# Kernel tuning notes

Measured on AMD Instinct MI355X. Metric: run time of the kernel, lower is better.

## Reference

```python
import jax, jax.numpy as jnp
import numpy as np

B, C, CI, H, W = 8, 256, 128, 64, 64
EPS = 1e-5

def conv1x1(x, w, b):
    # x: [B,C,H,W], w: [O,C], b: [O]
    return jnp.einsum('bchw,oc->bohw', x, w) + b[None, :, None, None]

def avgpool2(x):
    b, c, h, w = x.shape
    return x.reshape(b, c, h // 2, 2, w // 2, 2).mean(axis=(3, 5))

def setup_inputs() -> dict:
    key = jax.random.key(0)
    ks = jax.random.split(key, 16)
    s = lambda fan: 1.0 / np.sqrt(fan)
    inp = {
        'q': jax.random.normal(ks[0], (B, C, H, W), jnp.float32),
        'k': jax.random.normal(ks[1], (B, C, H, W), jnp.float32),
        'v': jax.random.normal(ks[2], (B, C, H, W), jnp.float32),
        'Wg':  jax.random.normal(ks[3], (CI, C), jnp.float32) * s(C),
        'bg':  jax.random.normal(ks[4], (CI,), jnp.float32) * s(C),
        'Wth': jax.random.normal(ks[5], (CI, C), jnp.float32) * s(C),
        'bth': jax.random.normal(ks[6], (CI,), jnp.float32) * s(C),
        'Wph': jax.random.normal(ks[7], (CI, C), jnp.float32) * s(C),
        'bph': jax.random.normal(ks[8], (CI,), jnp.float32) * s(C),
        'Ww':  jax.random.normal(ks[9], (C, CI), jnp.float32) * s(CI),
        'bw':  jax.random.normal(ks[10], (C,), jnp.float32) * s(CI),
        'gamma': jax.random.normal(ks[11], (C,), jnp.float32) * 0.1 + 1.0,
        'beta':  jax.random.normal(ks[12], (C,), jnp.float32) * 0.1,
        'mean':  jax.random.normal(ks[13], (C,), jnp.float32) * 0.1,
        'var':   jax.random.uniform(ks[14], (C,), jnp.float32, 0.5, 1.5),
    }
    return inp

def reference(q, k, v, Wg, bg, Wth, bth, Wph, bph, Ww, bw, gamma, beta, mean, var):
    b = q.shape[0]
    # g branch on v, phi branch on q: 1x1 conv then 2x2 avg-pool (sub_sample)
    g_x = avgpool2(conv1x1(v, Wg, bg)).reshape(b, CI, -1)            # [B,CI,M]
    g_x = g_x.transpose(0, 2, 1)                                      # [B,M,CI]
    theta_x = conv1x1(k, Wth, bth).reshape(b, CI, -1).transpose(0, 2, 1)  # [B,N,CI]
    phi_x = avgpool2(conv1x1(q, Wph, bph)).reshape(b, CI, -1)        # [B,CI,M]
    f = jnp.einsum('bnc,bcm->bnm', theta_x, phi_x)                   # [B,N,M]
    f_div_C = jax.nn.softmax(f, axis=-1)
    y = jnp.einsum('bnm,bmc->bnc', f_div_C, g_x)                     # [B,N,CI]
    y = y.transpose(0, 2, 1).reshape(b, CI, H, W)
    W_y = conv1x1(y, Ww, bw)
    # BatchNorm2d (inference form)
    W_y = (W_y - mean[None, :, None, None]) * (gamma[None, :, None, None]
            * jax.lax.rsqrt(var + EPS)[None, :, None, None]) + beta[None, :, None, None]
    return W_y + v
```

## Files before the change

### kernel.cpp

```cpp
#include <hip/hip_runtime.h>
#include <cstddef>

typedef unsigned short u16;
typedef unsigned int u32;
typedef __attribute__((ext_vector_type(8))) __bf16 bf16x8;
typedef __attribute__((ext_vector_type(4))) float f32x4;

constexpr int kB = 8, kC = 256, kCI = 128, kN = 4096, kM = 1024;
constexpr int kHM = 512;
constexpr int kCH = 32;
constexpr int kNCH = kHM / kCH;
constexpr float kEPS = 1e-5f;
constexpr float kLOG2E = 1.44269504088896f;

__device__ __forceinline__ u16 f2bf(float f) {
    u32 u = __float_as_uint(f);
    u32 r = (u + 0x7fffu + ((u >> 16) & 1u)) >> 16;
    return (u16)r;
}

__device__ __forceinline__ void gload_lds16(const u16* g, u16* l) {
    __builtin_amdgcn_global_load_lds(
        (const __attribute__((address_space(1))) void*)g,
        (__attribute__((address_space(3))) void*)l, 16, 0, 0);
}

__global__ __launch_bounds__(256) void prep_kernel(const float* __restrict__ Wth,
                                                   const float* __restrict__ bth,
                                                   const float* __restrict__ Wph,
                                                   const float* __restrict__ Wg,
                                                   const float* __restrict__ Ww,
                                                   const float* __restrict__ bw,
                                                   const float* __restrict__ gamma,
                                                   const float* __restrict__ beta,
                                                   const float* __restrict__ mean,
                                                   const float* __restrict__ var,
                                                   u16* __restrict__ Wthb,
                                                   u16* __restrict__ Wphb,
                                                   u16* __restrict__ Wgb,
                                                   u16* __restrict__ Wwsb,
                                                   float* __restrict__ bb,
                                                   float* __restrict__ bthl) {
    int idx = blockIdx.x * 256 + threadIdx.x;
    if (idx < 32768) {
        Wthb[idx] = f2bf(Wth[idx] * kLOG2E);
        if (idx < kCI) bthl[idx] = bth[idx] * kLOG2E;
    } else if (idx < 65536) {
        int j = idx - 32768; Wphb[j] = f2bf(Wph[j]);
    } else if (idx < 98304) {
        int j = idx - 65536; Wgb[j] = f2bf(Wg[j]);
    } else {
        int j = idx - 98304;
        int co = j >> 7;
        float sc = gamma[co] * rsqrtf(var[co] + kEPS);
        Wwsb[j] = f2bf(Ww[j] * sc);
        if ((j & 127) == 0) bb[co] = (bw[co] - mean[co]) * sc + beta[co];
    }
}

template <int POOL>
__device__ __forceinline__ void conv_body(const float* __restrict__ x,
                                          const u16* __restrict__ Wb,
                                          const float* __restrict__ bias,
                                          u16* __restrict__ out, int Mn,
                                          int cmajor, int b, int n0,
                                          u16* w_lds, u16* x_lds) {
    int t = threadIdx.x;
    int w = t >> 6, lane = t & 63, l15 = lane & 15, quad = lane >> 4;
    int xn = t & 63, cbb = (t >> 6) * 2;

    f32x4 acc[8];
#pragma unroll
    for (int i = 0; i < 8; i++) acc[i] = (f32x4){0.f, 0.f, 0.f, 0.f};

    for (int c0 = 0; c0 < kC; c0 += 64) {
        __syncthreads();
#pragma unroll
        for (int i = 0; i < 4; i++) {
            int u = t + 256 * i;
            int ci = u >> 3, blk = u & 7;
            *(uint4*)&w_lds[ci * 72 + blk * 8] =
                *(const uint4*)&Wb[ci * kC + c0 + blk * 8];
        }
#pragma unroll
        for (int cc = 0; cc < 2; cc++) {
            int cb = cbb + cc;
            float f[8];
            if (POOL) {
                int p = n0 + xn, ph_ = p >> 5, pw_ = p & 31;
#pragma unroll
                for (int j = 0; j < 8; j++) {
                    const float* src = x + ((size_t)(b * kC + c0 + cb * 8 + j) * 64
                                            + 2 * ph_) * 64 + 2 * pw_;
                    float2 a = *(const float2*)src;
                    float2 b2 = *(const float2*)(src + 64);
                    f[j] = 0.25f * (a.x + a.y + b2.x + b2.y);
                }
            } else {
#pragma unroll
                for (int j = 0; j < 8; j++)
                    f[j] = x[(size_t)(b * kC + c0 + cb * 8 + j) * Mn + n0 + xn];
            }
            uint4 pk;
            pk.x = (u32)f2bf(f[0]) | ((u32)f2bf(f[1]) << 16);
            pk.y = (u32)f2bf(f[2]) | ((u32)f2bf(f[3]) << 16);
            pk.z = (u32)f2bf(f[4]) | ((u32)f2bf(f[5]) << 16);
            pk.w = (u32)f2bf(f[6]) | ((u32)f2bf(f[7]) << 16);
            *(uint4*)&x_lds[xn * 64 + ((cb ^ (xn & 7)) * 8)] = pk;
        }
        __syncthreads();

#pragma unroll
        for (int ks = 0; ks < 2; ks++) {
            int px = w * 16 + l15;
            bf16x8 xf = *(const bf16x8*)&x_lds[px * 64 + (((ks * 4 + quad) ^ (px & 7)) * 8)];
#pragma unroll
            for (int ct = 0; ct < 8; ct++) {
                bf16x8 wf = *(const bf16x8*)&w_lds[(ct * 16 + l15) * 72 + ks * 32 + quad * 8];
                if (cmajor)
                    acc[ct] = __builtin_amdgcn_mfma_f32_16x16x32_bf16(xf, wf, acc[ct], 0, 0, 0);
                else
                    acc[ct] = __builtin_amdgcn_mfma_f32_16x16x32_bf16(wf, xf, acc[ct], 0, 0, 0);
            }
        }
    }

    if (cmajor == 0) {
        int px = n0 + w * 16 + l15;
#pragma unroll
        for (int ct = 0; ct < 8; ct++) {
            int ci0 = ct * 16 + quad * 4;
            uint2 pk;
            pk.x = (u32)f2bf(acc[ct][0] + bias[ci0 + 0]) |
                   ((u32)f2bf(acc[ct][1] + bias[ci0 + 1]) << 16);
            pk.y = (u32)f2bf(acc[ct][2] + bias[ci0 + 2]) |
                   ((u32)f2bf(acc[ct][3] + bias[ci0 + 3]) << 16);
            *(uint2*)&out[(size_t)(b * Mn + px) * kCI + ci0] = pk;
        }
    } else {
        int px = n0 + w * 16 + quad * 4;
#pragma unroll
        for (int ct = 0; ct < 8; ct++) {
            int ci = ct * 16 + l15;
            float bs = bias[ci];
            uint2 pk;
            pk.x = (u32)f2bf(acc[ct][0] + bs) | ((u32)f2bf(acc[ct][1] + bs) << 16);
            pk.y = (u32)f2bf(acc[ct][2] + bs) | ((u32)f2bf(acc[ct][3] + bs) << 16);
            *(uint2*)&out[(size_t)(b * kCI + ci) * Mn + px] = pk;
        }
    }
}

__global__ __launch_bounds__(256) void convs_kernel(const float* __restrict__ q,
                                                    const float* __restrict__ k,
                                                    const float* __restrict__ v,
                                                    const u16* __restrict__ Wthb,
                                                    const u16* __restrict__ Wphb,
                                                    const u16* __restrict__ Wgb,
                                                    const float* __restrict__ bthl,
                                                    const float* __restrict__ bph,
                                                    const float* __restrict__ bg,
                                                    u16* __restrict__ theta,
                                                    u16* __restrict__ phi,
                                                    u16* __restrict__ g) {
    __shared__ __align__(16) u16 w_lds[128 * 72];
    __shared__ __align__(16) u16 x_lds[64 * 64];
    int bx = blockIdx.x, b = blockIdx.y;
    if (bx < 64) {
        conv_body<0>(k, Wthb, bthl, theta, kN, 0, b, bx * 64, w_lds, x_lds);
    } else {
        int z = (bx >= 80);
        int n0 = (z ? (bx - 80) : (bx - 64)) * 64;
        conv_body<1>(z ? v : q, z ? Wgb : Wphb, z ? bg : bph, z ? g : phi,
                     kM, z, b, n0, w_lds, x_lds);
    }
}

__global__ __launch_bounds__(512, 4) void attn_kernel(const u16* __restrict__ theta,
                                                      const u16* __restrict__ phi,
                                                      const u16* __restrict__ g,
                                                      u16* __restrict__ y) {
    __shared__ __align__(16) u16 ph_lds[2][2][4096];
    __shared__ __align__(16) u16 p_lds[8 * 512];
    __shared__ float mlsh[128];

    int t = threadIdx.x, b = blockIdx.y, n0 = blockIdx.x * 64;
    int w = t >> 6, lane = t & 63, l15 = lane & 15, quad = lane >> 4;
    int half = w >> 2, wl = w & 3, th = t & 255;
    int sw = (l15 >> 1) & 3;

    bf16x8 thf[4];
    const u16* thB = theta + ((size_t)(b * kN) + n0 + wl * 16 + l15) * kCI;
#pragma unroll
    for (int ks = 0; ks < 4; ks++)
        thf[ks] = *(const bf16x8*)&thB[ks * 32 + quad * 8];

    f32x4 oacc[8];
#pragma unroll
    for (int ct = 0; ct < 8; ct++) oacc[ct] = (f32x4){0.f, 0.f, 0.f, 0.f};
    float m_ = -1e30f, l_ = 0.f;

    const u16* phB = phi + ((size_t)b * kM + half * kHM) * kCI;
    const u16* gB  = g + (size_t)b * kCI * kM + half * kHM;
    u16* pw = p_lds + w * 512;

    int m_st = (th >> 2) & 31;
    int kbx = (th & 3) ^ ((th >> 3) & 3);
    int go0 = m_st * kCI + kbx * 8 + (th >> 7) * 32;
    u16* dst0 = &ph_lds[half][0][wl * 512];

    {
        const u16* src = phB + go0;
        gload_lds16(src, dst0);
        gload_lds16(src + 64, dst0 + 2048);
    }

    for (int ch = 0; ch < kNCH; ++ch) {
        asm volatile("s_waitcnt vmcnt(0)" ::: "memory");
        __syncthreads();
        if (ch + 1 < kNCH) {
            const u16* src = phB + (ch + 1) * kCH * kCI + go0;
            u16* dst = &ph_lds[half][(ch + 1) & 1][wl * 512];
            gload_lds16(src, dst);
            gload_lds16(src + 64, dst + 2048);
        }
        const u16* buf = &ph_lds[half][ch & 1][0];

        f32x4 sacc[2];
#pragma unroll
        for (int mt = 0; mt < 2; mt++) sacc[mt] = (f32x4){0.f, 0.f, 0.f, 0.f};
#pragma unroll
        for (int ks = 0; ks < 4; ks++)
#pragma unroll
            for (int mt = 0; mt < 2; mt++) {
                bf16x8 a = *(const bf16x8*)&buf[ks * 1024 + (mt * 16 + l15) * 32 +
                                                ((quad ^ sw) * 8)];
                sacc[mt] = __builtin_amdgcn_mfma_f32_16x16x32_bf16(a, thf[ks], sacc[mt], 0, 0, 0);
            }

        float mc = -1e30f;
#pragma unroll
        for (int mt = 0; mt < 2; mt++)
#pragma unroll
            for (int r = 0; r < 4; r++) mc = fmaxf(mc, sacc[mt][r]);
        mc = fmaxf(mc, __shfl_xor(mc, 16, 64));
        mc = fmaxf(mc, __shfl_xor(mc, 32, 64));
        if (__any(mc > m_ + 8.0f)) {
            float mn = fmaxf(m_, mc);
            float al = exp2f(m_ - mn);
            m_ = mn;
            l_ *= al;
#pragma unroll
            for (int ct = 0; ct < 8; ct++)
#pragma unroll
                for (int r = 0; r < 4; r++) oacc[ct][r] *= al;
        }
        float rs = 0.f;
#pragma unroll
        for (int mt = 0; mt < 2; mt++)
#pragma unroll
            for (int r = 0; r < 4; r++) {
                float p = exp2f(sacc[mt][r] - m_);
                sacc[mt][r] = p;
                rs += p;
            }
        rs += __shfl_xor(rs, 16, 64);
        rs += __shfl_xor(rs, 32, 64);
        l_ += rs;

#pragma unroll
        for (int mt = 0; mt < 2; mt++)
#pragma unroll
            for (int h = 0; h < 2; h++) {
                u32 d = (u32)f2bf(sacc[mt][2 * h]) | ((u32)f2bf(sacc[mt][2 * h + 1]) << 16);
                int m = mt * 16 + quad * 4 + 2 * h;
                int kblk = (m >> 3) & 3;
                int j = (quad & 1) * 4 + 2 * h;
                *(u32*)&pw[l15 * 32 + ((kblk ^ sw) * 8) + j] = d;
            }

        const u16* gC = gB + ch * kCH;
        bf16x8 bfrag = *(const bf16x8*)&pw[l15 * 32 + ((quad ^ sw) * 8)];
#pragma unroll
        for (int ct = 0; ct < 8; ct++) {
            bf16x8 a = *(const bf16x8*)&gC[(size_t)(ct * 16 + l15) * kM + quad * 8];
            oacc[ct] = __builtin_amdgcn_mfma_f32_16x16x32_bf16(a, bfrag, oacc[ct], 0, 0, 0);
        }
    }

    __syncthreads();
    float* olds = (float*)&ph_lds[0][0][0];
    int nl = wl * 16 + l15;
    if (half == 1) {
#pragma unroll
        for (int ct = 0; ct < 8; ct++) {
            int s = (ct * 4 + quad) ^ (nl & 7);
            *(f32x4*)&olds[nl * 128 + s * 4] = oacc[ct];
        }
        if (quad == 0) { mlsh[2 * nl] = m_; mlsh[2 * nl + 1] = l_; }
    }
    __syncthreads();
    if (half == 0) {
        float m1 = mlsh[2 * nl], l1 = mlsh[2 * nl + 1];
        float mm = fmaxf(m_, m1);
        float w0 = exp2f(m_ - mm), w1 = exp2f(m1 - mm);
        float inv = 1.0f / (l_ * w0 + l1 * w1);
        float a0 = w0 * inv, a1 = w1 * inv;
        u16* yr = y + ((size_t)(b * kN) + n0 + nl) * kCI + quad * 4;
#pragma unroll
        for (int ct = 0; ct < 8; ct++) {
            int s = (ct * 4 + quad) ^ (nl & 7);
            f32x4 o1 = *(const f32x4*)&olds[nl * 128 + s * 4];
            uint2 pk;
            pk.x = (u32)f2bf(oacc[ct][0] * a0 + o1[0] * a1) |
                   ((u32)f2bf(oacc[ct][1] * a0 + o1[1] * a1) << 16);
            pk.y = (u32)f2bf(oacc[ct][2] * a0 + o1[2] * a1) |
                   ((u32)f2bf(oacc[ct][3] * a0 + o1[3] * a1) << 16);
            *(uint2*)&yr[ct * 16] = pk;
        }
    }
}

__global__ __launch_bounds__(256) void final_kernel(const u16* __restrict__ y,
                                                    const u16* __restrict__ Wws,
                                                    const float* __restrict__ bb,
                                                    const float* __restrict__ v,
                                                    float* __restrict__ out) {
    __shared__ __align__(16) u16 y_lds[64 * 136];
    int t = threadIdx.x, b = blockIdx.y, n0 = blockIdx.x * 64;
    int z = blockIdx.z;
    int w = t >> 6, lane = t & 63, l15 = lane & 15, quad = lane >> 4;

#pragma unroll
    for (int i = 0; i < 4; i++) {
        int u = t + 256 * i;
        int row = u >> 4, blk = u & 15;
        *(uint4*)&y_lds[row * 136 + blk * 8] =
            *(const uint4*)&y[(size_t)(b * kN + n0 + row) * kCI + blk * 8];
    }
    __syncthreads();

    bf16x8 af[4];
#pragma unroll
    for (int ks = 0; ks < 4; ks++)
        af[ks] = *(const bf16x8*)&y_lds[(w * 16 + l15) * 136 + ks * 32 + quad * 8];

#pragma unroll
    for (int ct = 0; ct < 8; ct++) {
        f32x4 a = (f32x4){0.f, 0.f, 0.f, 0.f};
        int co = z * 128 + ct * 16 + l15;
#pragma unroll
        for (int ks = 0; ks < 4; ks++) {
            bf16x8 bf = *(const bf16x8*)&Wws[(size_t)co * kCI + ks * 32 + quad * 8];
            a = __builtin_amdgcn_mfma_f32_16x16x32_bf16(af[ks], bf, a, 0, 0, 0);
        }
        float bbv = bb[co];
        size_t base = (size_t)(b * kC + co) * kN + n0 + w * 16 + quad * 4;
        float4 vv = *(const float4*)&v[base];
        float4 ov;
        ov.x = a[0] + bbv + vv.x;
        ov.y = a[1] + bbv + vv.y;
        ov.z = a[2] + bbv + vv.z;
        ov.w = a[3] + bbv + vv.w;
        *(float4*)&out[base] = ov;
    }
}

extern "C" void kernel_launch(void* const* d_in, const int* in_sizes, int n_in,
                              void* d_out, int out_size, void* d_ws, size_t ws_size,
                              hipStream_t stream) {
    (void)in_sizes; (void)n_in; (void)out_size; (void)ws_size;
    const float* q     = (const float*)d_in[0];
    const float* k     = (const float*)d_in[1];
    const float* v     = (const float*)d_in[2];
    const float* Wg    = (const float*)d_in[3];
    const float* bg    = (const float*)d_in[4];
    const float* Wth   = (const float*)d_in[5];
    const float* bth   = (const float*)d_in[6];
    const float* Wph   = (const float*)d_in[7];
    const float* bph   = (const float*)d_in[8];
    const float* Ww    = (const float*)d_in[9];
    const float* bw    = (const float*)d_in[10];
    const float* gamma = (const float*)d_in[11];
    const float* beta  = (const float*)d_in[12];
    const float* mean  = (const float*)d_in[13];
    const float* var   = (const float*)d_in[14];
    float* out = (float*)d_out;

    u16* wsu = (u16*)d_ws;
    u16*   theta = wsu;
    u16*   phi   = theta + 4194304;
    u16*   gbuf  = phi + 1048576;
    u16*   ybuf  = gbuf + 1048576;
    u16*   Wthb  = ybuf + 4194304;
    u16*   Wphb  = Wthb + 32768;
    u16*   Wgb   = Wphb + 32768;
    u16*   Wwsb  = Wgb + 32768;
    float* bbuf  = (float*)(Wwsb + 32768);
    float* bthl  = bbuf + 256;

    prep_kernel<<<dim3(512), 256, 0, stream>>>(Wth, bth, Wph, Wg, Ww, bw, gamma, beta,
                                               mean, var, Wthb, Wphb, Wgb, Wwsb,
                                               bbuf, bthl);
    convs_kernel<<<dim3(96, 8), 256, 0, stream>>>(q, k, v, Wthb, Wphb, Wgb,
                                                  bthl, bph, bg, theta, phi, gbuf);
    attn_kernel<<<dim3(64, 8), 512, 0, stream>>>(theta, phi, gbuf, ybuf);
    final_kernel<<<dim3(64, 8, 2), 256, 0, stream>>>(ybuf, Wwsb, bbuf, v, out);
}
```

Measured before the change: 252.4 us.

## Fold weight prep into conv/final kernels and double attention chunk size

Removes the separate prep kernel by converting fp32 weights to bf16 (with log2e and BatchNorm scaling) inline, inside the conv and final kernels. This drops one launch and its global round trip. It also raises the attention key chunk from 32 to 64 with matching LDS buffers and load mapping, so there are fewer sync and softmax-rescale iterations per chunk. The cost is redundant weight conversion in every block, a larger LDS footprint, and a BN scale now applied in fp32 after the MFMA instead of being folded into the bf16 weights.

New measurement: 275.0 us. 8.9% more time.

```diff
diff --git a/kernel.cpp b/kernel.cpp
--- a/kernel.cpp
+++ b/kernel.cpp
@@ -8,7 +8,7 @@
 
 constexpr int kB = 8, kC = 256, kCI = 128, kN = 4096, kM = 1024;
 constexpr int kHM = 512;
-constexpr int kCH = 32;
+constexpr int kCH = 64;
 constexpr int kNCH = kHM / kCH;
 constexpr float kEPS = 1e-5f;
 constexpr float kLOG2E = 1.44269504088896f;
@@ -25,43 +25,11 @@
         (__attribute__((address_space(3))) void*)l, 16, 0, 0);
 }
 
-__global__ __launch_bounds__(256) void prep_kernel(const float* __restrict__ Wth,
-                                                   const float* __restrict__ bth,
-                                                   const float* __restrict__ Wph,
-                                                   const float* __restrict__ Wg,
-                                                   const float* __restrict__ Ww,
-                                                   const float* __restrict__ bw,
-                                                   const float* __restrict__ gamma,
-                                                   const float* __restrict__ beta,
-                                                   const float* __restrict__ mean,
-                                                   const float* __restrict__ var,
-                                                   u16* __restrict__ Wthb,
-                                                   u16* __restrict__ Wphb,
-                                                   u16* __restrict__ Wgb,
-                                                   u16* __restrict__ Wwsb,
-                                                   float* __restrict__ bb,
-                                                   float* __restrict__ bthl) {
-    int idx = blockIdx.x * 256 + threadIdx.x;
-    if (idx < 32768) {
-        Wthb[idx] = f2bf(Wth[idx] * kLOG2E);
-        if (idx < kCI) bthl[idx] = bth[idx] * kLOG2E;
-    } else if (idx < 65536) {
-        int j = idx - 32768; Wphb[j] = f2bf(Wph[j]);
-    } else if (idx < 98304) {
-        int j = idx - 65536; Wgb[j] = f2bf(Wg[j]);
-    } else {
-        int j = idx - 98304;
-        int co = j >> 7;
-        float sc = gamma[co] * rsqrtf(var[co] + kEPS);
-        Wwsb[j] = f2bf(Ww[j] * sc);
-        if ((j & 127) == 0) bb[co] = (bw[co] - mean[co]) * sc + beta[co];
-    }
-}
-
 template <int POOL>
 __device__ __forceinline__ void conv_body(const float* __restrict__ x,
-                                          const u16* __restrict__ Wb,
+                                          const float* __restrict__ Wf,
                                           const float* __restrict__ bias,
+                                          float wscale, float bscale,
                                           u16* __restrict__ out, int Mn,
                                           int cmajor, int b, int n0,
                                           u16* w_lds, u16* x_lds) {
@@ -79,8 +47,15 @@
         for (int i = 0; i < 4; i++) {
             int u = t + 256 * i;
             int ci = u >> 3, blk = u & 7;
-            *(uint4*)&w_lds[ci * 72 + blk * 8] =
-                *(const uint4*)&Wb[ci * kC + c0 + blk * 8];
+            const float* ws = &Wf[ci * kC + c0 + blk * 8];
+            float4 wa = *(const float4*)ws;
+            float4 wb2 = *(const float4*)(ws + 4);
+            bf16x8 pk;
+            pk[0] = (__bf16)(wa.x * wscale);  pk[1] = (__bf16)(wa.y * wscale);
+            pk[2] = (__bf16)(wa.z * wscale);  pk[3] = (__bf16)(wa.w * wscale);
+            pk[4] = (__bf16)(wb2.x * wscale); pk[5] = (__bf16)(wb2.y * wscale);
+            pk[6] = (__bf16)(wb2.z * wscale); pk[7] = (__bf16)(wb2.w * wscale);
+            *(bf16x8*)&w_lds[ci * 72 + blk * 8] = pk;
         }
 #pragma unroll
         for (int cc = 0; cc < 2; cc++) {
@@ -131,10 +106,10 @@
         for (int ct = 0; ct < 8; ct++) {
             int ci0 = ct * 16 + quad * 4;
             uint2 pk;
-            pk.x = (u32)f2bf(acc[ct][0] + bias[ci0 + 0]) |
-                   ((u32)f2bf(acc[ct][1] + bias[ci0 + 1]) << 16);
-            pk.y = (u32)f2bf(acc[ct][2] + bias[ci0 + 2]) |
-                   ((u32)f2bf(acc[ct][3] + bias[ci0 + 3]) << 16);
+            pk.x = (u32)f2bf(acc[ct][0] + bias[ci0 + 0] * bscale) |
+                   ((u32)f2bf(acc[ct][1] + bias[ci0 + 1] * bscale) << 16);
+            pk.y = (u32)f2bf(acc[ct][2] + bias[ci0 + 2] * bscale) |
+                   ((u32)f2bf(acc[ct][3] + bias[ci0 + 3] * bscale) << 16);
             *(uint2*)&out[(size_t)(b * Mn + px) * kCI + ci0] = pk;
         }
     } else {
@@ -142,7 +117,7 @@
 #pragma unroll
         for (int ct = 0; ct < 8; ct++) {
             int ci = ct * 16 + l15;
-            float bs = bias[ci];
+            float bs = bias[ci] * bscale;
             uint2 pk;
             pk.x = (u32)f2bf(acc[ct][0] + bs) | ((u32)f2bf(acc[ct][1] + bs) << 16);
             pk.y = (u32)f2bf(acc[ct][2] + bs) | ((u32)f2bf(acc[ct][3] + bs) << 16);
@@ -154,10 +129,10 @@
 __global__ __launch_bounds__(256) void convs_kernel(const float* __restrict__ q,
                                                     const float* __restrict__ k,
                                                     const float* __restrict__ v,
-                                                    const u16* __restrict__ Wthb,
-                                                    const u16* __restrict__ Wphb,
-                                                    const u16* __restrict__ Wgb,
-                                                    const float* __restrict__ bthl,
+                                                    const float* __restrict__ Wth,
+                                                    const float* __restrict__ Wph,
+                                                    const float* __restrict__ Wg,
+                                                    const float* __restrict__ bth,
                                                     const float* __restrict__ bph,
                                                     const float* __restrict__ bg,
                                                     u16* __restrict__ theta,
@@ -167,12 +142,13 @@
     __shared__ __align__(16) u16 x_lds[64 * 64];
     int bx = blockIdx.x, b = blockIdx.y;
     if (bx < 64) {
-        conv_body<0>(k, Wthb, bthl, theta, kN, 0, b, bx * 64, w_lds, x_lds);
+        conv_body<0>(k, Wth, bth, kLOG2E, kLOG2E, theta, kN, 0, b, bx * 64,
+                     w_lds, x_lds);
     } else {
         int z = (bx >= 80);
         int n0 = (z ? (bx - 80) : (bx - 64)) * 64;
-        conv_body<1>(z ? v : q, z ? Wgb : Wphb, z ? bg : bph, z ? g : phi,
-                     kM, z, b, n0, w_lds, x_lds);
+        conv_body<1>(z ? v : q, z ? Wg : Wph, z ? bg : bph, 1.0f, 1.0f,
+                     z ? g : phi, kM, z, b, n0, w_lds, x_lds);
     }
 }
 
@@ -180,7 +156,7 @@
                                                       const u16* __restrict__ phi,
                                                       const u16* __restrict__ g,
                                                       u16* __restrict__ y) {
-    __shared__ __align__(16) u16 ph_lds[2][2][4096];
+    __shared__ __align__(16) u16 ph_lds[2][2][8192];
     __shared__ __align__(16) u16 p_lds[8 * 512];
     __shared__ float mlsh[128];
 
@@ -204,43 +180,45 @@
     const u16* gB  = g + (size_t)b * kCI * kM + half * kHM;
     u16* pw = p_lds + w * 512;
 
-    int m_st = (th >> 2) & 31;
-    int kbx = (th & 3) ^ ((th >> 3) & 3);
-    int go0 = m_st * kCI + kbx * 8 + (th >> 7) * 32;
-    u16* dst0 = &ph_lds[half][0][wl * 512];
-
-    {
-        const u16* src = phB + go0;
-        gload_lds16(src, dst0);
-        gload_lds16(src + 64, dst0 + 2048);
-    }
+    int go_[4];
+#pragma unroll
+    for (int i = 0; i < 4; i++) {
+        int W = th + 256 * i;
+        int ks = W >> 8, m = (W >> 2) & 63, slot = W & 3;
+        go_[i] = m * kCI + (((ks << 2) | (slot ^ ((m >> 1) & 3))) * 8);
+    }
+
+#pragma unroll
+    for (int i = 0; i < 4; i++)
+        gload_lds16(phB + go_[i], &ph_lds[half][0][(wl * 64 + 256 * i) * 8]);
 
     for (int ch = 0; ch < kNCH; ++ch) {
         asm volatile("s_waitcnt vmcnt(0)" ::: "memory");
         __syncthreads();
         if (ch + 1 < kNCH) {
-            const u16* src = phB + (ch + 1) * kCH * kCI + go0;
-            u16* dst = &ph_lds[half][(ch + 1) & 1][wl * 512];
-            gload_lds16(src, dst);
-            gload_lds16(src + 64, dst + 2048);
+            const u16* src = phB + (ch + 1) * kCH * kCI;
+            u16* dbuf = &ph_lds[half][(ch + 1) & 1][0];
+#pragma unroll
+            for (int i = 0; i < 4; i++)
+                gload_lds16(src + go_[i], &dbuf[(wl * 64 + 256 * i) * 8]);
         }
         const u16* buf = &ph_lds[half][ch & 1][0];
 
-        f32x4 sacc[2];
-#pragma unroll
-        for (int mt = 0; mt < 2; mt++) sacc[mt] = (f32x4){0.f, 0.f, 0.f, 0.f};
+        f32x4 sacc[4];
+#pragma unroll
+        for (int mt = 0; mt < 4; mt++) sacc[mt] = (f32x4){0.f, 0.f, 0.f, 0.f};
 #pragma unroll
         for (int ks = 0; ks < 4; ks++)
 #pragma unroll
-            for (int mt = 0; mt < 2; mt++) {
-                bf16x8 a = *(const bf16x8*)&buf[ks * 1024 + (mt * 16 + l15) * 32 +
+            for (int mt = 0; mt < 4; mt++) {
+                bf16x8 a = *(const bf16x8*)&buf[ks * 2048 + (mt * 16 + l15) * 32 +
                                                 ((quad ^ sw) * 8)];
                 sacc[mt] = __builtin_amdgcn_mfma_f32_16x16x32_bf16(a, thf[ks], sacc[mt], 0, 0, 0);
             }
 
         float mc = -1e30f;
 #pragma unroll
-        for (int mt = 0; mt < 2; mt++)
+        for (int mt = 0; mt < 4; mt++)
 #pragma unroll
             for (int r = 0; r < 4; r++) mc = fmaxf(mc, sacc[mt][r]);
         mc = fmaxf(mc, __shfl_xor(mc, 16, 64));
@@ -257,7 +235,7 @@
         }
         float rs = 0.f;
 #pragma unroll
-        for (int mt = 0; mt < 2; mt++)
+        for (int mt = 0; mt < 4; mt++)
 #pragma unroll
             for (int r = 0; r < 4; r++) {
                 float p = exp2f(sacc[mt][r] - m_);
@@ -268,23 +246,29 @@
         rs += __shfl_xor(rs, 32, 64);
         l_ += rs;
 
-#pragma unroll
-        for (int mt = 0; mt < 2; mt++)
-#pragma unroll
-            for (int h = 0; h < 2; h++) {
-                u32 d = (u32)f2bf(sacc[mt][2 * h]) | ((u32)f2bf(sacc[mt][2 * h + 1]) << 16);
-                int m = mt * 16 + quad * 4 + 2 * h;
-                int kblk = (m >> 3) & 3;
-                int j = (quad & 1) * 4 + 2 * h;
-                *(u32*)&pw[l15 * 32 + ((kblk ^ sw) * 8) + j] = d;
-            }
-
         const u16* gC = gB + ch * kCH;
-        bf16x8 bfrag = *(const bf16x8*)&pw[l15 * 32 + ((quad ^ sw) * 8)];
-#pragma unroll
-        for (int ct = 0; ct < 8; ct++) {
-            bf16x8 a = *(const bf16x8*)&gC[(size_t)(ct * 16 + l15) * kM + quad * 8];
-            oacc[ct] = __builtin_amdgcn_mfma_f32_16x16x32_bf16(a, bfrag, oacc[ct], 0, 0, 0);
+#pragma unroll
+        for (int ks2 = 0; ks2 < 2; ks2++) {
+#pragma unroll
+            for (int mh = 0; mh < 2; mh++) {
+                int mt = ks2 * 2 + mh;
+#pragma unroll
+                for (int h = 0; h < 2; h++) {
+                    u32 d = (u32)f2bf(sacc[mt][2 * h]) |
+                            ((u32)f2bf(sacc[mt][2 * h + 1]) << 16);
+                    int m = mt * 16 + quad * 4 + 2 * h;
+                    int kblk = (m >> 3) & 3;
+                    int j = (quad & 1) * 4 + 2 * h;
+                    *(u32*)&pw[l15 * 32 + ((kblk ^ sw) * 8) + j] = d;
+                }
+            }
+            bf16x8 bfrag = *(const bf16x8*)&pw[l15 * 32 + ((quad ^ sw) * 8)];
+#pragma unroll
+            for (int ct = 0; ct < 8; ct++) {
+                bf16x8 a = *(const bf16x8*)&gC[(size_t)(ct * 16 + l15) * kM +
+                                               ks2 * 32 + quad * 8];
+                oacc[ct] = __builtin_amdgcn_mfma_f32_16x16x32_bf16(a, bfrag, oacc[ct], 0, 0, 0);
+            }
         }
     }
 
@@ -322,8 +306,12 @@
 }
 
 __global__ __launch_bounds__(256) void final_kernel(const u16* __restrict__ y,
-                                                    const u16* __restrict__ Wws,
-                                                    const float* __restrict__ bb,
+                                                    const float* __restrict__ Ww,
+                                                    const float* __restrict__ gamma,
+                                                    const float* __restrict__ beta,
+                                                    const float* __restrict__ mean,
+                                                    const float* __restrict__ var,
+                                                    const float* __restrict__ bw,
                                                     const float* __restrict__ v,
                                                     float* __restrict__ out) {
     __shared__ __align__(16) u16 y_lds[64 * 136];
@@ -347,21 +335,29 @@
 
 #pragma unroll
     for (int ct = 0; ct < 8; ct++) {
+        int co = z * 128 + ct * 16 + l15;
         f32x4 a = (f32x4){0.f, 0.f, 0.f, 0.f};
-        int co = z * 128 + ct * 16 + l15;
 #pragma unroll
         for (int ks = 0; ks < 4; ks++) {
-            bf16x8 bf = *(const bf16x8*)&Wws[(size_t)co * kCI + ks * 32 + quad * 8];
+            const float* ws = &Ww[(size_t)co * kCI + ks * 32 + quad * 8];
+            float4 wa = *(const float4*)ws;
+            float4 wb2 = *(const float4*)(ws + 4);
+            bf16x8 bf;
+            bf[0] = (__bf16)wa.x;  bf[1] = (__bf16)wa.y;
+            bf[2] = (__bf16)wa.z;  bf[3] = (__bf16)wa.w;
+            bf[4] = (__bf16)wb2.x; bf[5] = (__bf16)wb2.y;
+            bf[6] = (__bf16)wb2.z; bf[7] = (__bf16)wb2.w;
             a = __builtin_amdgcn_mfma_f32_16x16x32_bf16(af[ks], bf, a, 0, 0, 0);
         }
-        float bbv = bb[co];
+        float sc = gamma[co] * rsqrtf(var[co] + kEPS);
+        float bbv = (bw[co] - mean[co]) * sc + beta[co];
         size_t base = (size_t)(b * kC + co) * kN + n0 + w * 16 + quad * 4;
         float4 vv = *(const float4*)&v[base];
         float4 ov;
-        ov.x = a[0] + bbv + vv.x;
-        ov.y = a[1] + bbv + vv.y;
-        ov.z = a[2] + bbv + vv.z;
-        ov.w = a[3] + bbv + vv.w;
+        ov.x = a[0] * sc + bbv + vv.x;
+        ov.y = a[1] * sc + bbv + vv.y;
+        ov.z = a[2] * sc + bbv + vv.z;
+        ov.w = a[3] * sc + bbv + vv.w;
         *(float4*)&out[base] = ov;
     }
 }
@@ -388,22 +384,14 @@
     float* out = (float*)d_out;
 
     u16* wsu = (u16*)d_ws;
-    u16*   theta = wsu;
-    u16*   phi   = theta + 4194304;
-    u16*   gbuf  = phi + 1048576;
-    u16*   ybuf  = gbuf + 1048576;
-    u16*   Wthb  = ybuf + 4194304;
-    u16*   Wphb  = Wthb + 32768;
-    u16*   Wgb   = Wphb + 32768;
-    u16*   Wwsb  = Wgb + 32768;
-    float* bbuf  = (float*)(Wwsb + 32768);
-    float* bthl  = bbuf + 256;
-
-    prep_kernel<<<dim3(512), 256, 0, stream>>>(Wth, bth, Wph, Wg, Ww, bw, gamma, beta,
-                                               mean, var, Wthb, Wphb, Wgb, Wwsb,
-                                               bbuf, bthl);
-    convs_kernel<<<dim3(96, 8), 256, 0, stream>>>(q, k, v, Wthb, Wphb, Wgb,
-                                                  bthl, bph, bg, theta, phi, gbuf);
+    u16* theta = wsu;
+    u16* phi   = theta + 4194304;
+    u16* gbuf  = phi + 1048576;
+    u16* ybuf  = gbuf + 1048576;
+
+    convs_kernel<<<dim3(96, 8), 256, 0, stream>>>(q, k, v, Wth, Wph, Wg,
+                                                  bth, bph, bg, theta, phi, gbuf);
     attn_kernel<<<dim3(64, 8), 512, 0, stream>>>(theta, phi, gbuf, ybuf);
-    final_kernel<<<dim3(64, 8, 2), 256, 0, stream>>>(ybuf, Wwsb, bbuf, v, out);
-}
+    final_kernel<<<dim3(64, 8, 2), 256, 0, stream>>>(ybuf, Ww, gamma, beta,
+                                                     mean, var, bw, v, out);
+}
```

## Restructure attention to 4 waves over full M with software-pipelined QK/softmax

Applied to the files above, without the earlier changes.

The attention kernel drops the two-halves split over M, which needed 8 waves and an LDS merge of partial softmax states. Each of 4 waves now processes all of M in chunks of 64 with ping-pong LDS buffers. The QK MFMA for the next chunk is issued before the softmax and PV of the current chunk so that matrix work overlaps the exp and bf16 conversion. The per-chunk row-sum shuffles move to a single reduction at the end. In exchange, each block runs half as many waves with twice as many serial iterations, so occupancy and latency hiding may drop.

Result: slower. 266.1 us (+5.4%).

```diff
diff --git a/kernel.cpp b/kernel.cpp
--- a/kernel.cpp
+++ b/kernel.cpp
@@ -7,9 +7,8 @@
 typedef __attribute__((ext_vector_type(4))) float f32x4;
 
 constexpr int kB = 8, kC = 256, kCI = 128, kN = 4096, kM = 1024;
-constexpr int kHM = 512;
-constexpr int kCH = 32;
-constexpr int kNCH = kHM / kCH;
+constexpr int kCH = 64;
+constexpr int kNCH = kM / kCH;
 constexpr float kEPS = 1e-5f;
 constexpr float kLOG2E = 1.44269504088896f;
 
@@ -176,21 +175,19 @@
     }
 }
 
-__global__ __launch_bounds__(512, 4) void attn_kernel(const u16* __restrict__ theta,
+__global__ __launch_bounds__(256, 2) void attn_kernel(const u16* __restrict__ theta,
                                                       const u16* __restrict__ phi,
                                                       const u16* __restrict__ g,
                                                       u16* __restrict__ y) {
-    __shared__ __align__(16) u16 ph_lds[2][2][4096];
-    __shared__ __align__(16) u16 p_lds[8 * 512];
-    __shared__ float mlsh[128];
+    __shared__ __align__(16) u16 ph_lds[2][8192];
+    __shared__ __align__(16) u16 p_lds[4 * 512];
 
     int t = threadIdx.x, b = blockIdx.y, n0 = blockIdx.x * 64;
     int w = t >> 6, lane = t & 63, l15 = lane & 15, quad = lane >> 4;
-    int half = w >> 2, wl = w & 3, th = t & 255;
     int sw = (l15 >> 1) & 3;
 
     bf16x8 thf[4];
-    const u16* thB = theta + ((size_t)(b * kN) + n0 + wl * 16 + l15) * kCI;
+    const u16* thB = theta + ((size_t)(b * kN) + n0 + w * 16 + l15) * kCI;
 #pragma unroll
     for (int ks = 0; ks < 4; ks++)
         thf[ks] = *(const bf16x8*)&thB[ks * 32 + quad * 8];
@@ -200,47 +197,43 @@
     for (int ct = 0; ct < 8; ct++) oacc[ct] = (f32x4){0.f, 0.f, 0.f, 0.f};
     float m_ = -1e30f, l_ = 0.f;
 
-    const u16* phB = phi + ((size_t)b * kM + half * kHM) * kCI;
-    const u16* gB  = g + (size_t)b * kCI * kM + half * kHM;
+    const u16* phB = phi + (size_t)b * kM * kCI;
+    const u16* gB  = g + (size_t)b * kCI * kM;
     u16* pw = p_lds + w * 512;
 
-    int m_st = (th >> 2) & 31;
-    int kbx = (th & 3) ^ ((th >> 3) & 3);
-    int go0 = m_st * kCI + kbx * 8 + (th >> 7) * 32;
-    u16* dst0 = &ph_lds[half][0][wl * 512];
-
-    {
-        const u16* src = phB + go0;
-        gload_lds16(src, dst0);
-        gload_lds16(src + 64, dst0 + 2048);
-    }
-
-    for (int ch = 0; ch < kNCH; ++ch) {
-        asm volatile("s_waitcnt vmcnt(0)" ::: "memory");
-        __syncthreads();
-        if (ch + 1 < kNCH) {
-            const u16* src = phB + (ch + 1) * kCH * kCI + go0;
-            u16* dst = &ph_lds[half][(ch + 1) & 1][wl * 512];
-            gload_lds16(src, dst);
-            gload_lds16(src + 64, dst + 2048);
-        }
-        const u16* buf = &ph_lds[half][ch & 1][0];
-
-        f32x4 sacc[2];
-#pragma unroll
-        for (int mt = 0; mt < 2; mt++) sacc[mt] = (f32x4){0.f, 0.f, 0.f, 0.f};
+    int go_[4];
+#pragma unroll
+    for (int i = 0; i < 4; i++) {
+        int W = t + 256 * i;
+        int ks = W >> 8, m = (W >> 2) & 63, slot = W & 3;
+        go_[i] = m * kCI + (((ks << 2) | (slot ^ ((m >> 1) & 3))) * 8);
+    }
+
+    auto STAGE = [&](int buf, int ch) {
+        const u16* src = phB + ch * kCH * kCI;
+#pragma unroll
+        for (int i = 0; i < 4; i++)
+            gload_lds16(src + go_[i], &ph_lds[buf][(w * 64 + 256 * i) * 8]);
+    };
+
+    auto QK = [&](f32x4 (&sacc)[4], int buf) {
+#pragma unroll
+        for (int mt = 0; mt < 4; mt++) sacc[mt] = (f32x4){0.f, 0.f, 0.f, 0.f};
+        const u16* bufp = &ph_lds[buf][0];
 #pragma unroll
         for (int ks = 0; ks < 4; ks++)
 #pragma unroll
-            for (int mt = 0; mt < 2; mt++) {
-                bf16x8 a = *(const bf16x8*)&buf[ks * 1024 + (mt * 16 + l15) * 32 +
-                                                ((quad ^ sw) * 8)];
+            for (int mt = 0; mt < 4; mt++) {
+                bf16x8 a = *(const bf16x8*)&bufp[ks * 2048 + (mt * 16 + l15) * 32 +
+                                                 ((quad ^ sw) * 8)];
                 sacc[mt] = __builtin_amdgcn_mfma_f32_16x16x32_bf16(a, thf[ks], sacc[mt], 0, 0, 0);
             }
-
+    };
+
+    auto SMPV = [&](f32x4 (&sacc)[4], int ch) {
         float mc = -1e30f;
 #pragma unroll
-        for (int mt = 0; mt < 2; mt++)
+        for (int mt = 0; mt < 4; mt++)
 #pragma unroll
             for (int r = 0; r < 4; r++) mc = fmaxf(mc, sacc[mt][r]);
         mc = fmaxf(mc, __shfl_xor(mc, 16, 64));
@@ -257,67 +250,73 @@
         }
         float rs = 0.f;
 #pragma unroll
-        for (int mt = 0; mt < 2; mt++)
+        for (int mt = 0; mt < 4; mt++)
 #pragma unroll
             for (int r = 0; r < 4; r++) {
                 float p = exp2f(sacc[mt][r] - m_);
                 sacc[mt][r] = p;
                 rs += p;
             }
-        rs += __shfl_xor(rs, 16, 64);
-        rs += __shfl_xor(rs, 32, 64);
         l_ += rs;
 
-#pragma unroll
-        for (int mt = 0; mt < 2; mt++)
-#pragma unroll
-            for (int h = 0; h < 2; h++) {
-                u32 d = (u32)f2bf(sacc[mt][2 * h]) | ((u32)f2bf(sacc[mt][2 * h + 1]) << 16);
-                int m = mt * 16 + quad * 4 + 2 * h;
-                int kblk = (m >> 3) & 3;
-                int j = (quad & 1) * 4 + 2 * h;
-                *(u32*)&pw[l15 * 32 + ((kblk ^ sw) * 8) + j] = d;
-            }
-
         const u16* gC = gB + ch * kCH;
-        bf16x8 bfrag = *(const bf16x8*)&pw[l15 * 32 + ((quad ^ sw) * 8)];
-#pragma unroll
-        for (int ct = 0; ct < 8; ct++) {
-            bf16x8 a = *(const bf16x8*)&gC[(size_t)(ct * 16 + l15) * kM + quad * 8];
-            oacc[ct] = __builtin_amdgcn_mfma_f32_16x16x32_bf16(a, bfrag, oacc[ct], 0, 0, 0);
-        }
-    }
-
+#pragma unroll
+        for (int ks2 = 0; ks2 < 2; ks2++) {
+#pragma unroll
+            for (int mh = 0; mh < 2; mh++) {
+                int mt = ks2 * 2 + mh;
+#pragma unroll
+                for (int h = 0; h < 2; h++) {
+                    u32 d = (u32)f2bf(sacc[mt][2 * h]) |
+                            ((u32)f2bf(sacc[mt][2 * h + 1]) << 16);
+                    int m = mt * 16 + quad * 4 + 2 * h;
+                    int kblk = (m >> 3) & 3;
+                    int j = (quad & 1) * 4 + 2 * h;
+                    *(u32*)&pw[l15 * 32 + ((kblk ^ sw) * 8) + j] = d;
+                }
+            }
+            bf16x8 bfrag = *(const bf16x8*)&pw[l15 * 32 + ((quad ^ sw) * 8)];
+#pragma unroll
+            for (int ct = 0; ct < 8; ct++) {
+                bf16x8 a = *(const bf16x8*)&gC[(size_t)(ct * 16 + l15) * kM +
+                                               ks2 * 32 + quad * 8];
+                oacc[ct] = __builtin_amdgcn_mfma_f32_16x16x32_bf16(a, bfrag, oacc[ct], 0, 0, 0);
+            }
+        }
+    };
+
+    f32x4 sA[4], sB[4];
+
+    STAGE(0, 0);
+    asm volatile("s_waitcnt vmcnt(0)" ::: "memory");
     __syncthreads();
-    float* olds = (float*)&ph_lds[0][0][0];
-    int nl = wl * 16 + l15;
-    if (half == 1) {
-#pragma unroll
-        for (int ct = 0; ct < 8; ct++) {
-            int s = (ct * 4 + quad) ^ (nl & 7);
-            *(f32x4*)&olds[nl * 128 + s * 4] = oacc[ct];
-        }
-        if (quad == 0) { mlsh[2 * nl] = m_; mlsh[2 * nl + 1] = l_; }
-    }
-    __syncthreads();
-    if (half == 0) {
-        float m1 = mlsh[2 * nl], l1 = mlsh[2 * nl + 1];
-        float mm = fmaxf(m_, m1);
-        float w0 = exp2f(m_ - mm), w1 = exp2f(m1 - mm);
-        float inv = 1.0f / (l_ * w0 + l1 * w1);
-        float a0 = w0 * inv, a1 = w1 * inv;
-        u16* yr = y + ((size_t)(b * kN) + n0 + nl) * kCI + quad * 4;
-#pragma unroll
-        for (int ct = 0; ct < 8; ct++) {
-            int s = (ct * 4 + quad) ^ (nl & 7);
-            f32x4 o1 = *(const f32x4*)&olds[nl * 128 + s * 4];
-            uint2 pk;
-            pk.x = (u32)f2bf(oacc[ct][0] * a0 + o1[0] * a1) |
-                   ((u32)f2bf(oacc[ct][1] * a0 + o1[1] * a1) << 16);
-            pk.y = (u32)f2bf(oacc[ct][2] * a0 + o1[2] * a1) |
-                   ((u32)f2bf(oacc[ct][3] * a0 + o1[3] * a1) << 16);
-            *(uint2*)&yr[ct * 16] = pk;
-        }
+    STAGE(1, 1);
+    QK(sA, 0);
+
+    for (int c = 0; c < kNCH; c += 2) {
+        asm volatile("s_waitcnt vmcnt(0)" ::: "memory");
+        __syncthreads();
+        if (c + 2 < kNCH) STAGE(0, c + 2);
+        QK(sB, 1);
+        SMPV(sA, c);
+        asm volatile("s_waitcnt vmcnt(0)" ::: "memory");
+        __syncthreads();
+        if (c + 3 < kNCH) STAGE(1, c + 3);
+        if (c + 2 < kNCH) QK(sA, 0);
+        SMPV(sB, c + 1);
+    }
+
+    l_ += __shfl_xor(l_, 16, 64);
+    l_ += __shfl_xor(l_, 32, 64);
+    float inv = 1.0f / l_;
+    int n = n0 + w * 16 + l15;
+    u16* yr = y + ((size_t)(b * kN) + n) * kCI + quad * 4;
+#pragma unroll
+    for (int ct = 0; ct < 8; ct++) {
+        uint2 pk;
+        pk.x = (u32)f2bf(oacc[ct][0] * inv) | ((u32)f2bf(oacc[ct][1] * inv) << 16);
+        pk.y = (u32)f2bf(oacc[ct][2] * inv) | ((u32)f2bf(oacc[ct][3] * inv) << 16);
+        *(uint2*)&yr[ct * 16] = pk;
     }
 }
 
@@ -347,8 +346,8 @@
 
 #pragma unroll
     for (int ct = 0; ct < 8; ct++) {
+        int co = z * 128 + ct * 16 + l15;
         f32x4 a = (f32x4){0.f, 0.f, 0.f, 0.f};
-        int co = z * 128 + ct * 16 + l15;
 #pragma unroll
         for (int ks = 0; ks < 4; ks++) {
             bf16x8 bf = *(const bf16x8*)&Wws[(size_t)co * kCI + ks * 32 + quad * 8];
@@ -404,6 +403,6 @@
                                                bbuf, bthl);
     convs_kernel<<<dim3(96, 8), 256, 0, stream>>>(q, k, v, Wthb, Wphb, Wgb,
                                                   bthl, bph, bg, theta, phi, gbuf);
-    attn_kernel<<<dim3(64, 8), 512, 0, stream>>>(theta, phi, gbuf, ybuf);
+    attn_kernel<<<dim3(64, 8), 256, 0, stream>>>(theta, phi, gbuf, ybuf);
     final_kernel<<<dim3(64, 8, 2), 256, 0, stream>>>(ybuf, Wwsb, bbuf, v, out);
 }
```
